# Optimization experiments

Measured on AMD Instinct MI355X. Metric: run time of the kernel, lower is better.

## Reference

```python
import jax, jax.numpy as jnp
import numpy as np

B, S, D = 4, 2048, 1024
H = 16
HD = D // H  # 64


def setup_inputs() -> dict:
    key = jax.random.key(0)
    ks = jax.random.split(key, 6)
    s = 0.02
    return {
        "x": jax.random.normal(ks[0], (B, S, D), dtype=jnp.float32),
        "w_q": jax.random.normal(ks[1], (D, D), dtype=jnp.float32) * s,
        "w_k": jax.random.normal(ks[2], (D, D), dtype=jnp.float32) * s,
        "w_v": jax.random.normal(ks[3], (D, D), dtype=jnp.float32) * s,
        "w_o": jax.random.normal(ks[4], (D, D), dtype=jnp.float32) * s,
        "b_o": jnp.zeros((D,), dtype=jnp.float32),
    }


def reference(x, w_q, w_k, w_v, w_o, b_o):
    b, n, d_in = x.shape
    # QKV projections (torch Linear: y = x @ W^T), reshape to heads
    q = (x @ w_q.T).reshape(b, n, H, HD).transpose(0, 2, 1, 3)  # [b,h,n,hd]
    k = (x @ w_k.T).reshape(b, n, H, HD).transpose(0, 2, 1, 3)
    v = (x @ w_v.T).reshape(b, n, H, HD).transpose(0, 2, 1, 3)
    scores = jnp.einsum("bhqd,bhkd->bhqk", q, k)
    causal = jnp.triu(jnp.ones((n, n), dtype=bool), k=1)  # True above diagonal -> masked
    scores = jnp.where(causal, -jnp.inf, scores)
    attn = jax.nn.softmax(scores / jnp.sqrt(jnp.float32(HD)), axis=-1)
    # dropout p=0.0 (no-op)
    ctx = jnp.einsum("bhqk,bhkd->bhqd", attn, v)
    ctx = ctx.transpose(0, 2, 1, 3).reshape(b, n, D)
    return ctx @ w_o.T + b_o
```

## Files before the change

### kernel.cpp

```cpp
#include <hip/hip_runtime.h>
#include <hip/hip_bf16.h>

typedef __bf16 bf16x8 __attribute__((ext_vector_type(8)));
typedef float f32x4 __attribute__((ext_vector_type(4)));
typedef unsigned short u16x4 __attribute__((ext_vector_type(4)));
typedef unsigned short u16x8 __attribute__((ext_vector_type(8)));

__device__ __forceinline__ unsigned short f2bf(float f) {
  unsigned int u = __float_as_uint(f);
  u += 0x7FFFu + ((u >> 16) & 1u);
  return (unsigned short)(u >> 16);
}

__device__ __forceinline__ float exp2_fast(float x) {
  return __builtin_amdgcn_exp2f(x);
}

__device__ __forceinline__ void gld_lds16(const void* g, void* l) {
  __builtin_amdgcn_global_load_lds(
      (__attribute__((address_space(1))) void*)g,
      (__attribute__((address_space(3))) void*)l,
      16, 0, 0);
}

__global__ __launch_bounds__(256)
void cvt_bf16(const float* __restrict__ x, const float* __restrict__ wq,
              const float* __restrict__ wk, const float* __restrict__ wv,
              const float* __restrict__ wo,
              unsigned short* __restrict__ Xb, unsigned short* __restrict__ Wb)
{
  unsigned c = blockIdx.x * 256 + threadIdx.x;
  const float* src;
  unsigned short* dst;
  unsigned off;
  if (c < 1048576u) {
    src = x; dst = Xb; off = c;
  } else {
    unsigned cc = c - 1048576u;
    unsigned which = cc >> 17;
    off = cc & 131071u;
    src = which == 0 ? wq : which == 1 ? wk : which == 2 ? wv : wo;
    dst = Wb + (size_t)which * 1048576u;
  }
  f32x4 a = *reinterpret_cast<const f32x4*>(src + (size_t)off * 8);
  f32x4 b = *reinterpret_cast<const f32x4*>(src + (size_t)off * 8 + 4);
  u16x8 o = {f2bf(a.x), f2bf(a.y), f2bf(a.z), f2bf(a.w),
             f2bf(b.x), f2bf(b.y), f2bf(b.z), f2bf(b.w)};
  *reinterpret_cast<u16x8*>(dst + (size_t)off * 8) = o;
}

__global__ __launch_bounds__(256, 3)
void qkv_proj_b(const unsigned short* __restrict__ Xb, const unsigned short* __restrict__ Wb,
                unsigned short* __restrict__ Qb, unsigned short* __restrict__ Kb,
                unsigned short* __restrict__ Vb)
{
  __shared__ __align__(16) unsigned short As[128 * 64];
  __shared__ __align__(16) unsigned short Bs[128 * 64];
  char* AsB = (char*)As;
  char* BsB = (char*)Bs;

  const int z = blockIdx.z;
  const unsigned short* __restrict__ W = Wb + (size_t)z * 1048576u;
  unsigned short* __restrict__ Out = (z == 0) ? Qb : (z == 1) ? Kb : Vb;

  const int flat = blockIdx.x + (blockIdx.y << 3);
  const int swz = (flat & 7) * 64 + (flat >> 3);
  const int n0 = (swz & 7) * 128;
  const int m0 = (swz >> 3) * 128;

  const int t = threadIdx.x;
  const int lane = t & 63, wid = t >> 6;
  const int wr = wid >> 1, wc = wid & 1;
  const int l15 = lane & 15, g = lane >> 4;

  f32x4 acc[4][4] = {};

  for (int kt = 0; kt < 1024; kt += 64) {
#pragma unroll
    for (int i = 0; i < 4; ++i) {
      const int rbase = wid * 32 + i * 8;
      const int row = rbase + (lane >> 3);
      const int swzb = ((lane & 7) * 16) ^ ((row & 7) << 4);
      gld_lds16((const char*)Xb + ((size_t)(m0 + row) * 1024 + kt) * 2 + swzb,
                AsB + rbase * 128);
      gld_lds16((const char*)W + ((size_t)(n0 + row) * 1024 + kt) * 2 + swzb,
                BsB + rbase * 128);
    }
    __syncthreads();

#pragma unroll
    for (int ks = 0; ks < 2; ++ks) {
      const int kpre = ks * 64 + g * 16;
      bf16x8 af[4], bfr[4];
#pragma unroll
      for (int mi = 0; mi < 4; ++mi) {
        int row = wr * 64 + mi * 16 + l15;
        af[mi] = *reinterpret_cast<const bf16x8*>(AsB + row * 128 + (kpre ^ ((row & 7) << 4)));
      }
#pragma unroll
      for (int ni = 0; ni < 4; ++ni) {
        int row = wc * 64 + ni * 16 + l15;
        bfr[ni] = *reinterpret_cast<const bf16x8*>(BsB + row * 128 + (kpre ^ ((row & 7) << 4)));
      }
#pragma unroll
      for (int mi = 0; mi < 4; ++mi)
#pragma unroll
        for (int ni = 0; ni < 4; ++ni)
          acc[mi][ni] = __builtin_amdgcn_mfma_f32_16x16x32_bf16(af[mi], bfr[ni], acc[mi][ni], 0, 0, 0);
    }
    __syncthreads();
  }

  if (z == 2) {
#pragma unroll
    for (int mi = 0; mi < 4; ++mi)
#pragma unroll
      for (int ni = 0; ni < 4; ++ni) {
        int n = n0 + wc * 64 + ni * 16 + l15;
        int h = n >> 6, hd = n & 63;
        int m = m0 + wr * 64 + mi * 16 + 4 * g;
        int b = m >> 11, s0 = m & 2047;
        u16x4 pk = {f2bf(acc[mi][ni][0]), f2bf(acc[mi][ni][1]),
                    f2bf(acc[mi][ni][2]), f2bf(acc[mi][ni][3])};
        *reinterpret_cast<u16x4*>(Out + ((size_t)(b * 16 + h) * 64 + hd) * 2048 + s0) = pk;
      }
  } else {
    const float qs = (z == 0) ? 0.1803368801f : 1.0f;
#pragma unroll
    for (int mi = 0; mi < 4; ++mi)
#pragma unroll
      for (int ni = 0; ni < 4; ++ni)
#pragma unroll
        for (int r = 0; r < 4; ++r) {
          int m = m0 + wr * 64 + mi * 16 + 4 * g + r;
          int n = n0 + wc * 64 + ni * 16 + l15;
          int b = m >> 11, s = m & 2047;
          int h = n >> 6, hd = n & 63;
          Out[((size_t)(b * 16 + h) * 2048 + s) * 64 + hd] = f2bf(acc[mi][ni][r] * qs);
        }
  }
}

__global__ __launch_bounds__(256, 3)
void out_proj_b(const unsigned short* __restrict__ Ctx, const unsigned short* __restrict__ Wob,
                const float* __restrict__ Bo, float* __restrict__ Y)
{
  __shared__ __align__(16) unsigned short As[128 * 64];
  __shared__ __align__(16) unsigned short Bs[128 * 64];
  char* AsB = (char*)As;
  char* BsB = (char*)Bs;

  const int flat = blockIdx.x + (blockIdx.y << 3);
  const int swz = (flat & 7) * 64 + (flat >> 3);
  const int n0 = (swz & 7) * 128;
  const int m0 = (swz >> 3) * 128;

  const int t = threadIdx.x;
  const int lane = t & 63, wid = t >> 6;
  const int wr = wid >> 1, wc = wid & 1;
  const int l15 = lane & 15, g = lane >> 4;

  f32x4 acc[4][4] = {};

  for (int kt = 0; kt < 1024; kt += 64) {
#pragma unroll
    for (int i = 0; i < 4; ++i) {
      const int rbase = wid * 32 + i * 8;
      const int row = rbase + (lane >> 3);
      const int swzb = ((lane & 7) * 16) ^ ((row & 7) << 4);
      gld_lds16((const char*)Ctx + ((size_t)(m0 + row) * 1024 + kt) * 2 + swzb,
                AsB + rbase * 128);
      gld_lds16((const char*)Wob + ((size_t)(n0 + row) * 1024 + kt) * 2 + swzb,
                BsB + rbase * 128);
    }
    __syncthreads();

#pragma unroll
    for (int ks = 0; ks < 2; ++ks) {
      const int kpre = ks * 64 + g * 16;
      bf16x8 af[4], bfr[4];
#pragma unroll
      for (int mi = 0; mi < 4; ++mi) {
        int row = wr * 64 + mi * 16 + l15;
        af[mi] = *reinterpret_cast<const bf16x8*>(AsB + row * 128 + (kpre ^ ((row & 7) << 4)));
      }
#pragma unroll
      for (int ni = 0; ni < 4; ++ni) {
        int row = wc * 64 + ni * 16 + l15;
        bfr[ni] = *reinterpret_cast<const bf16x8*>(BsB + row * 128 + (kpre ^ ((row & 7) << 4)));
      }
#pragma unroll
      for (int mi = 0; mi < 4; ++mi)
#pragma unroll
        for (int ni = 0; ni < 4; ++ni)
          acc[mi][ni] = __builtin_amdgcn_mfma_f32_16x16x32_bf16(af[mi], bfr[ni], acc[mi][ni], 0, 0, 0);
    }
    __syncthreads();
  }

#pragma unroll
  for (int mi = 0; mi < 4; ++mi)
#pragma unroll
    for (int ni = 0; ni < 4; ++ni) {
      int n = n0 + wc * 64 + ni * 16 + l15;
      float bias = Bo[n];
#pragma unroll
      for (int r = 0; r < 4; ++r) {
        int m = m0 + wr * 64 + mi * 16 + 4 * g + r;
        Y[(size_t)m * 1024 + n] = acc[mi][ni][r] + bias;
      }
    }
}

__global__ __launch_bounds__(256, 2)
void attn4(const unsigned short* __restrict__ Qb, const unsigned short* __restrict__ Kb,
           const unsigned short* __restrict__ Vtg, unsigned short* __restrict__ Ctx)
{
  __shared__ __align__(16) unsigned short Ks[2][64 * 64];
  __shared__ __align__(16) unsigned short Vts[2][64 * 64];
  __shared__ __align__(16) unsigned short Pl[4][64 * 64];

  const int flat = blockIdx.x;
  const int xcd = flat & 7;
  const int idx = flat >> 3;
  const int bh = xcd * 8 + (idx >> 3);
  const int tile = 7 - (idx & 7);

  const size_t base = (size_t)bh * (2048 * 64);
  const int lane = threadIdx.x & 63, wid = threadIdx.x >> 6;
  const int l15 = lane & 15, g = lane >> 4;
  char* PB = (char*)Pl[wid];
  const int bb = bh >> 4, hh = bh & 15;

  const int sl8 = lane >> 3;
  const int sc8 = lane & 7;
  const int pswz = (l15 & 7) << 4;

  const int qg0 = tile * 256 + wid * 64;
  const int nst = 4 * (tile + 1);

  bf16x8 qf[4][2];
#pragma unroll
  for (int mi = 0; mi < 4; ++mi)
#pragma unroll
    for (int ks = 0; ks < 2; ++ks)
      qf[mi][ks] = *reinterpret_cast<const bf16x8*>(
          Qb + base + (size_t)(qg0 + 16 * mi + l15) * 64 + ks * 32 + g * 8);

  bf16x8 ones;
#pragma unroll
  for (int i = 0; i < 8; ++i) ones[i] = (__bf16)1.0f;

  f32x4 o[4][4] = {};
  f32x4 accl[4] = {};

#pragma unroll
  for (int i = 0; i < 2; ++i) {
    int row = wid * 16 + i * 8 + sl8;
    int swzb = (sc8 * 16) ^ ((row & 7) << 4);
    gld_lds16((const char*)Kb + (base + (size_t)row * 64) * 2 + swzb,
              (char*)Ks[0] + (wid * 16 + i * 8) * 128);
    gld_lds16((const char*)Vtg + (base + (size_t)row * 2048) * 2 + swzb,
              (char*)Vts[0] + (wid * 16 + i * 8) * 128);
  }
  __syncthreads();

  int cur = 0;
  for (int s = 0; s < nst; ++s) {
    if (s + 1 < nst) {
#pragma unroll
      for (int i = 0; i < 2; ++i) {
        int row = wid * 16 + i * 8 + sl8;
        int swzb = (sc8 * 16) ^ ((row & 7) << 4);
        gld_lds16((const char*)Kb + (base + (size_t)((s + 1) * 64 + row) * 64) * 2 + swzb,
                  (char*)Ks[cur ^ 1] + (wid * 16 + i * 8) * 128);
        gld_lds16((const char*)Vtg + (base + (size_t)row * 2048 + (s + 1) * 64) * 2 + swzb,
                  (char*)Vts[cur ^ 1] + (wid * 16 + i * 8) * 128);
      }
    }
    char* KsB = (char*)Ks[cur];
    char* VtB = (char*)Vts[cur];

    f32x4 sw[4][4] = {};
#pragma unroll
    for (int ks = 0; ks < 2; ++ks) {
      const int kpre = ks * 64 + g * 16;
#pragma unroll
      for (int ni = 0; ni < 4; ++ni) {
        int row = ni * 16 + l15;
        bf16x8 kf = *reinterpret_cast<const bf16x8*>(KsB + row * 128 + (kpre ^ ((row & 7) << 4)));
#pragma unroll
        for (int mi = 0; mi < 4; ++mi)
          sw[mi][ni] = __builtin_amdgcn_mfma_f32_16x16x32_bf16(kf, qf[mi][ks], sw[mi][ni], 0, 0, 0);
      }
    }

    const bool needmask = (s * 64 + 63 > qg0);
    const int dgl = s * 64 + 4 * g - l15 - qg0;
#pragma unroll
    for (int mi = 0; mi < 4; ++mi) {
#pragma unroll
      for (int ni = 0; ni < 4; ++ni) {
        f32x4 v = sw[mi][ni];
        if (needmask) {
          int dbase = dgl + 16 * ni - 16 * mi;
#pragma unroll
          for (int r = 0; r < 4; ++r)
            if (dbase + r > 0) v[r] = -1e30f;
        }
        float p0 = exp2_fast(v[0]);
        float p1 = exp2_fast(v[1]);
        float p2 = exp2_fast(v[2]);
        float p3 = exp2_fast(v[3]);
        uint2 w;
        w.x = (__float_as_uint(p0) >> 16) | (__float_as_uint(p1) & 0xFFFF0000u);
        w.y = (__float_as_uint(p2) >> 16) | (__float_as_uint(p3) & 0xFFFF0000u);
        *reinterpret_cast<uint2*>(PB + (16 * mi + l15) * 128 + ((32 * ni + 8 * g) ^ pswz)) = w;
      }
    }
    asm volatile("s_waitcnt lgkmcnt(0)" ::: "memory");
    __builtin_amdgcn_sched_barrier(0);

#pragma unroll
    for (int ks2 = 0; ks2 < 2; ++ks2) {
      const int kpre = ks2 * 64 + g * 16;
      bf16x8 pa[4];
#pragma unroll
      for (int mi = 0; mi < 4; ++mi) {
        pa[mi] = *reinterpret_cast<const bf16x8*>(PB + (16 * mi + l15) * 128 + (kpre ^ pswz));
        accl[mi] = __builtin_amdgcn_mfma_f32_16x16x32_bf16(ones, pa[mi], accl[mi], 0, 0, 0);
      }
#pragma unroll
      for (int db = 0; db < 4; ++db) {
        int vrow = db * 16 + l15;
        bf16x8 vf = *reinterpret_cast<const bf16x8*>(VtB + vrow * 128 + (kpre ^ ((vrow & 7) << 4)));
#pragma unroll
        for (int mi = 0; mi < 4; ++mi)
          o[mi][db] = __builtin_amdgcn_mfma_f32_16x16x32_bf16(vf, pa[mi], o[mi][db], 0, 0, 0);
      }
    }
    __syncthreads();
    cur ^= 1;
  }

#pragma unroll
  for (int mi = 0; mi < 4; ++mi) {
    float inv = 1.0f / accl[mi][0];
    int qg = qg0 + 16 * mi + l15;
#pragma unroll
    for (int db = 0; db < 4; ++db) {
      u16x4 pk = {f2bf(o[mi][db][0] * inv), f2bf(o[mi][db][1] * inv),
                  f2bf(o[mi][db][2] * inv), f2bf(o[mi][db][3] * inv)};
      *reinterpret_cast<u16x4*>(Ctx + ((size_t)(bb * 2048 + qg)) * 1024 + hh * 64 + db * 16 + 4 * g) = pk;
    }
  }
}

__global__ __launch_bounds__(256, 2)
void qkv_proj(const float* __restrict__ X,
              const float* __restrict__ Wq, const float* __restrict__ Wk,
              const float* __restrict__ Wv,
              unsigned short* __restrict__ Qb, unsigned short* __restrict__ Kb,
              unsigned short* __restrict__ Vb)
{
  __shared__ __align__(16) unsigned short As[128 * 64];
  __shared__ __align__(16) unsigned short Bs[128 * 64];
  char* AsB = (char*)As;
  char* BsB = (char*)Bs;

  const float* __restrict__ W =
      (blockIdx.z == 0) ? Wq : (blockIdx.z == 1) ? Wk : Wv;
  unsigned short* __restrict__ Out =
      (blockIdx.z == 0) ? Qb : (blockIdx.z == 1) ? Kb : Vb;

  const int m0 = blockIdx.y * 128;
  const int n0 = blockIdx.x * 128;
  const int t = threadIdx.x;
  const int lane = t & 63, wid = t >> 6;
  const int wr = wid >> 1, wc = wid & 1;
  const int l15 = lane & 15, g = lane >> 4;

  f32x4 acc[4][4] = {};

  for (int kt = 0; kt < 1024; kt += 64) {
#pragma unroll
    for (int i = 0; i < 8; ++i) {
      int c = i * 256 + t;
      int row = c >> 4, c4 = c & 15;
      f32x4 a = *reinterpret_cast<const f32x4*>(X + (size_t)(m0 + row) * 1024 + kt + c4 * 4);
      f32x4 b = *reinterpret_cast<const f32x4*>(W + (size_t)(n0 + row) * 1024 + kt + c4 * 4);
      u16x4 va = {f2bf(a.x), f2bf(a.y), f2bf(a.z), f2bf(a.w)};
      u16x4 vb = {f2bf(b.x), f2bf(b.y), f2bf(b.z), f2bf(b.w)};
      int off = row * 128 + ((c4 * 8) ^ ((row & 7) << 4));
      *reinterpret_cast<u16x4*>(AsB + off) = va;
      *reinterpret_cast<u16x4*>(BsB + off) = vb;
    }
    __syncthreads();

#pragma unroll
    for (int ks = 0; ks < 2; ++ks) {
      const int kpre = ks * 64 + g * 16;
      bf16x8 af[4], bfr[4];
#pragma unroll
      for (int mi = 0; mi < 4; ++mi) {
        int row = wr * 64 + mi * 16 + l15;
        af[mi] = *reinterpret_cast<const bf16x8*>(AsB + row * 128 + (kpre ^ ((row & 7) << 4)));
      }
#pragma unroll
      for (int ni = 0; ni < 4; ++ni) {
        int row = wc * 64 + ni * 16 + l15;
        bfr[ni] = *reinterpret_cast<const bf16x8*>(BsB + row * 128 + (kpre ^ ((row & 7) << 4)));
      }
#pragma unroll
      for (int mi = 0; mi < 4; ++mi)
#pragma unroll
        for (int ni = 0; ni < 4; ++ni)
          acc[mi][ni] = __builtin_amdgcn_mfma_f32_16x16x32_bf16(af[mi], bfr[ni], acc[mi][ni], 0, 0, 0);
    }
    __syncthreads();
  }

  if (blockIdx.z == 2) {
#pragma unroll
    for (int mi = 0; mi < 4; ++mi)
#pragma unroll
      for (int ni = 0; ni < 4; ++ni) {
        int n = n0 + wc * 64 + ni * 16 + l15;
        int h = n >> 6, hd = n & 63;
        int m = m0 + wr * 64 + mi * 16 + 4 * g;
        int b = m >> 11, s0 = m & 2047;
        u16x4 pk = {f2bf(acc[mi][ni][0]), f2bf(acc[mi][ni][1]),
                    f2bf(acc[mi][ni][2]), f2bf(acc[mi][ni][3])};
        *reinterpret_cast<u16x4*>(Out + ((size_t)(b * 16 + h) * 64 + hd) * 2048 + s0) = pk;
      }
  } else {
    const float qs = (blockIdx.z == 0) ? 0.1803368801f : 1.0f;
#pragma unroll
    for (int mi = 0; mi < 4; ++mi)
#pragma unroll
      for (int ni = 0; ni < 4; ++ni)
#pragma unroll
        for (int r = 0; r < 4; ++r) {
          int m = m0 + wr * 64 + mi * 16 + 4 * g + r;
          int n = n0 + wc * 64 + ni * 16 + l15;
          int b = m >> 11, s = m & 2047;
          int h = n >> 6, hd = n & 63;
          Out[((size_t)(b * 16 + h) * 2048 + s) * 64 + hd] = f2bf(acc[mi][ni][r] * qs);
        }
  }
}

__global__ __launch_bounds__(256, 2)
void out_proj(const unsigned short* __restrict__ Ctx, const float* __restrict__ Wo,
              const float* __restrict__ Bo, float* __restrict__ Y)
{
  __shared__ __align__(16) unsigned short As[128 * 64];
  __shared__ __align__(16) unsigned short Bs[128 * 64];
  char* AsB = (char*)As;
  char* BsB = (char*)Bs;

  const int m0 = blockIdx.y * 128;
  const int n0 = blockIdx.x * 128;
  const int t = threadIdx.x;
  const int lane = t & 63, wid = t >> 6;
  const int wr = wid >> 1, wc = wid & 1;
  const int l15 = lane & 15, g = lane >> 4;

  f32x4 acc[4][4] = {};

  for (int kt = 0; kt < 1024; kt += 64) {
#pragma unroll
    for (int i = 0; i < 4; ++i) {
      int c = i * 256 + t;
      int row = c >> 3, c8 = c & 7;
      bf16x8 v = *reinterpret_cast<const bf16x8*>(Ctx + (size_t)(m0 + row) * 1024 + kt + c8 * 8);
      *reinterpret_cast<bf16x8*>(AsB + row * 128 + ((c8 * 16) ^ ((row & 7) << 4))) = v;
    }
#pragma unroll
    for (int i = 0; i < 8; ++i) {
      int c = i * 256 + t;
      int row = c >> 4, c4 = c & 15;
      f32x4 b = *reinterpret_cast<const f32x4*>(Wo + (size_t)(n0 + row) * 1024 + kt + c4 * 4);
      u16x4 vb = {f2bf(b.x), f2bf(b.y), f2bf(b.z), f2bf(b.w)};
      *reinterpret_cast<u16x4*>(BsB + row * 128 + ((c4 * 8) ^ ((row & 7) << 4))) = vb;
    }
    __syncthreads();

#pragma unroll
    for (int ks = 0; ks < 2; ++ks) {
      const int kpre = ks * 64 + g * 16;
      bf16x8 af[4], bfr[4];
#pragma unroll
      for (int mi = 0; mi < 4; ++mi) {
        int row = wr * 64 + mi * 16 + l15;
        af[mi] = *reinterpret_cast<const bf16x8*>(AsB + row * 128 + (kpre ^ ((row & 7) << 4)));
      }
#pragma unroll
      for (int ni = 0; ni < 4; ++ni) {
        int row = wc * 64 + ni * 16 + l15;
        bfr[ni] = *reinterpret_cast<const bf16x8*>(BsB + row * 128 + (kpre ^ ((row & 7) << 4)));
      }
#pragma unroll
      for (int mi = 0; mi < 4; ++mi)
#pragma unroll
        for (int ni = 0; ni < 4; ++ni)
          acc[mi][ni] = __builtin_amdgcn_mfma_f32_16x16x32_bf16(af[mi], bfr[ni], acc[mi][ni], 0, 0, 0);
    }
    __syncthreads();
  }

#pragma unroll
  for (int mi = 0; mi < 4; ++mi)
#pragma unroll
    for (int ni = 0; ni < 4; ++ni) {
      int n = n0 + wc * 64 + ni * 16 + l15;
      float bias = Bo[n];
#pragma unroll
      for (int r = 0; r < 4; ++r) {
        int m = m0 + wr * 64 + mi * 16 + 4 * g + r;
        Y[(size_t)m * 1024 + n] = acc[mi][ni][r] + bias;
      }
    }
}

extern "C" void kernel_launch(void* const* d_in, const int* in_sizes, int n_in,
                              void* d_out, int out_size, void* d_ws, size_t ws_size,
                              hipStream_t stream)
{
  const float* x  = (const float*)d_in[0];
  const float* wq = (const float*)d_in[1];
  const float* wk = (const float*)d_in[2];
  const float* wv = (const float*)d_in[3];
  const float* wo = (const float*)d_in[4];
  const float* bo = (const float*)d_in[5];
  float* y = (float*)d_out;

  if (ws_size >= 75497472ULL) {
    unsigned short* Xb = (unsigned short*)d_ws;
    unsigned short* Qb = Xb + 8388608;
    unsigned short* Kb = Qb + 8388608;
    unsigned short* Vb = Kb + 8388608;
    unsigned short* Wb = Vb + 8388608;
    unsigned short* Cx = Xb;

    cvt_bf16<<<6144, 256, 0, stream>>>(x, wq, wk, wv, wo, Xb, Wb);
    qkv_proj_b<<<dim3(8, 64, 3), 256, 0, stream>>>(Xb, Wb, Qb, Kb, Vb);
    attn4<<<512, 256, 0, stream>>>(Qb, Kb, Vb, Cx);
    out_proj_b<<<dim3(8, 64), 256, 0, stream>>>(Cx, Wb + 3 * 1048576, bo, y);
  } else {
    unsigned short* Qb = (unsigned short*)d_ws;
    unsigned short* Kb = Qb + 8388608;
    unsigned short* Vb = Kb + 8388608;
    unsigned short* Cx = Vb + 8388608;

    qkv_proj<<<dim3(8, 64, 3), 256, 0, stream>>>(x, wq, wk, wv, Qb, Kb, Vb);
    attn4<<<512, 256, 0, stream>>>(Qb, Kb, Vb, Cx);
    out_proj<<<dim3(8, 64), 256, 0, stream>>>(Cx, wo, bo, y);
  }
}
```

Baseline: 185.8 us.

## Pair causal query tiles per block to balance attention work

```diff
diff --git a/kernel.cpp b/kernel.cpp
--- a/kernel.cpp
+++ b/kernel.cpp
@@ -14,6 +14,10 @@
 
 __device__ __forceinline__ float exp2_fast(float x) {
   return __builtin_amdgcn_exp2f(x);
+}
+
+__device__ __forceinline__ unsigned pack_bf16(float lo, float hi) {
+  return __builtin_amdgcn_perm(__float_as_uint(hi), __float_as_uint(lo), 0x07060302u);
 }
 
 __device__ __forceinline__ void gld_lds16(const void* g, void* l) {
@@ -213,21 +217,22 @@
 }
 
 __global__ __launch_bounds__(256, 2)
-void attn4(const unsigned short* __restrict__ Qb, const unsigned short* __restrict__ Kb,
+void attn2(const unsigned short* __restrict__ Qb, const unsigned short* __restrict__ Kb,
            const unsigned short* __restrict__ Vtg, unsigned short* __restrict__ Ctx)
 {
   __shared__ __align__(16) unsigned short Ks[2][64 * 64];
   __shared__ __align__(16) unsigned short Vts[2][64 * 64];
-  __shared__ __align__(16) unsigned short Pl[4][64 * 64];
+  __shared__ __align__(16) unsigned short Pl[4][32 * 64];
 
   const int flat = blockIdx.x;
   const int xcd = flat & 7;
   const int idx = flat >> 3;
   const int bh = xcd * 8 + (idx >> 3);
-  const int tile = 7 - (idx & 7);
+  const int pr = idx & 7;
 
   const size_t base = (size_t)bh * (2048 * 64);
-  const int lane = threadIdx.x & 63, wid = threadIdx.x >> 6;
+  const int t = threadIdx.x;
+  const int lane = t & 63, wid = t >> 6;
   const int l15 = lane & 15, g = lane >> 4;
   char* PB = (char*)Pl[wid];
   const int bb = bh >> 4, hh = bh & 15;
@@ -236,122 +241,121 @@
   const int sc8 = lane & 7;
   const int pswz = (l15 & 7) << 4;
 
-  const int qg0 = tile * 256 + wid * 64;
-  const int nst = 4 * (tile + 1);
-
-  bf16x8 qf[4][2];
-#pragma unroll
-  for (int mi = 0; mi < 4; ++mi)
-#pragma unroll
-    for (int ks = 0; ks < 2; ++ks)
-      qf[mi][ks] = *reinterpret_cast<const bf16x8*>(
-          Qb + base + (size_t)(qg0 + 16 * mi + l15) * 64 + ks * 32 + g * 8);
-
   bf16x8 ones;
 #pragma unroll
   for (int i = 0; i < 8; ++i) ones[i] = (__bf16)1.0f;
 
-  f32x4 o[4][4] = {};
-  f32x4 accl[4] = {};
-
-#pragma unroll
-  for (int i = 0; i < 2; ++i) {
-    int row = wid * 16 + i * 8 + sl8;
-    int swzb = (sc8 * 16) ^ ((row & 7) << 4);
-    gld_lds16((const char*)Kb + (base + (size_t)row * 64) * 2 + swzb,
-              (char*)Ks[0] + (wid * 16 + i * 8) * 128);
-    gld_lds16((const char*)Vtg + (base + (size_t)row * 2048) * 2 + swzb,
-              (char*)Vts[0] + (wid * 16 + i * 8) * 128);
-  }
-  __syncthreads();
-
-  int cur = 0;
-  for (int s = 0; s < nst; ++s) {
-    if (s + 1 < nst) {
-#pragma unroll
-      for (int i = 0; i < 2; ++i) {
-        int row = wid * 16 + i * 8 + sl8;
-        int swzb = (sc8 * 16) ^ ((row & 7) << 4);
-        gld_lds16((const char*)Kb + (base + (size_t)((s + 1) * 64 + row) * 64) * 2 + swzb,
-                  (char*)Ks[cur ^ 1] + (wid * 16 + i * 8) * 128);
-        gld_lds16((const char*)Vtg + (base + (size_t)row * 2048 + (s + 1) * 64) * 2 + swzb,
-                  (char*)Vts[cur ^ 1] + (wid * 16 + i * 8) * 128);
-      }
-    }
-    char* KsB = (char*)Ks[cur];
-    char* VtB = (char*)Vts[cur];
-
-    f32x4 sw[4][4] = {};
-#pragma unroll
-    for (int ks = 0; ks < 2; ++ks) {
-      const int kpre = ks * 64 + g * 16;
-#pragma unroll
-      for (int ni = 0; ni < 4; ++ni) {
-        int row = ni * 16 + l15;
-        bf16x8 kf = *reinterpret_cast<const bf16x8*>(KsB + row * 128 + (kpre ^ ((row & 7) << 4)));
-#pragma unroll
-        for (int mi = 0; mi < 4; ++mi)
-          sw[mi][ni] = __builtin_amdgcn_mfma_f32_16x16x32_bf16(kf, qf[mi][ks], sw[mi][ni], 0, 0, 0);
-      }
-    }
-
-    const bool needmask = (s * 64 + 63 > qg0);
-    const int dgl = s * 64 + 4 * g - l15 - qg0;
-#pragma unroll
-    for (int mi = 0; mi < 4; ++mi) {
-#pragma unroll
-      for (int ni = 0; ni < 4; ++ni) {
-        f32x4 v = sw[mi][ni];
-        if (needmask) {
-          int dbase = dgl + 16 * ni - 16 * mi;
-#pragma unroll
-          for (int r = 0; r < 4; ++r)
-            if (dbase + r > 0) v[r] = -1e30f;
+  for (int half = 0; half < 2; ++half) {
+    const int tile = half ? (15 - pr) : pr;
+    const int qg0 = tile * 128 + wid * 32;
+    const int nst = 2 * tile + 2;
+
+    bf16x8 qf[2][2];
+#pragma unroll
+    for (int mi = 0; mi < 2; ++mi)
+#pragma unroll
+      for (int ks = 0; ks < 2; ++ks)
+        qf[mi][ks] = *reinterpret_cast<const bf16x8*>(
+            Qb + base + (size_t)(qg0 + 16 * mi + l15) * 64 + ks * 32 + g * 8);
+
+    f32x4 o[2][4] = {};
+    f32x4 accl[2] = {};
+
+#pragma unroll
+    for (int i = 0; i < 2; ++i) {
+      int row = wid * 16 + i * 8 + sl8;
+      int swzb = (sc8 * 16) ^ ((row & 7) << 4);
+      gld_lds16((const char*)Kb + (base + (size_t)row * 64) * 2 + swzb,
+                (char*)Ks[0] + (wid * 16 + i * 8) * 128);
+      gld_lds16((const char*)Vtg + (base + (size_t)row * 2048) * 2 + swzb,
+                (char*)Vts[0] + (wid * 16 + i * 8) * 128);
+    }
+    __syncthreads();
+
+    int cur = 0;
+    for (int s = 0; s < nst; ++s) {
+      if (s + 1 < nst) {
+#pragma unroll
+        for (int i = 0; i < 2; ++i) {
+          int row = wid * 16 + i * 8 + sl8;
+          int swzb = (sc8 * 16) ^ ((row & 7) << 4);
+          gld_lds16((const char*)Kb + (base + (size_t)((s + 1) * 64 + row) * 64) * 2 + swzb,
+                    (char*)Ks[cur ^ 1] + (wid * 16 + i * 8) * 128);
+          gld_lds16((const char*)Vtg + (base + (size_t)row * 2048 + (s + 1) * 64) * 2 + swzb,
+                    (char*)Vts[cur ^ 1] + (wid * 16 + i * 8) * 128);
         }
-        float p0 = exp2_fast(v[0]);
-        float p1 = exp2_fast(v[1]);
-        float p2 = exp2_fast(v[2]);
-        float p3 = exp2_fast(v[3]);
-        uint2 w;
-        w.x = (__float_as_uint(p0) >> 16) | (__float_as_uint(p1) & 0xFFFF0000u);
-        w.y = (__float_as_uint(p2) >> 16) | (__float_as_uint(p3) & 0xFFFF0000u);
-        *reinterpret_cast<uint2*>(PB + (16 * mi + l15) * 128 + ((32 * ni + 8 * g) ^ pswz)) = w;
-      }
-    }
-    asm volatile("s_waitcnt lgkmcnt(0)" ::: "memory");
-    __builtin_amdgcn_sched_barrier(0);
-
-#pragma unroll
-    for (int ks2 = 0; ks2 < 2; ++ks2) {
-      const int kpre = ks2 * 64 + g * 16;
-      bf16x8 pa[4];
-#pragma unroll
-      for (int mi = 0; mi < 4; ++mi) {
-        pa[mi] = *reinterpret_cast<const bf16x8*>(PB + (16 * mi + l15) * 128 + (kpre ^ pswz));
-        accl[mi] = __builtin_amdgcn_mfma_f32_16x16x32_bf16(ones, pa[mi], accl[mi], 0, 0, 0);
-      }
+      }
+      char* KsB = (char*)Ks[cur];
+      char* VtB = (char*)Vts[cur];
+
+      f32x4 sw[2][4] = {};
+#pragma unroll
+      for (int ks = 0; ks < 2; ++ks) {
+        const int kpre = ks * 64 + g * 16;
+#pragma unroll
+        for (int ni = 0; ni < 4; ++ni) {
+          int row = ni * 16 + l15;
+          bf16x8 kf = *reinterpret_cast<const bf16x8*>(KsB + row * 128 + (kpre ^ ((row & 7) << 4)));
+          sw[0][ni] = __builtin_amdgcn_mfma_f32_16x16x32_bf16(kf, qf[0][ks], sw[0][ni], 0, 0, 0);
+          sw[1][ni] = __builtin_amdgcn_mfma_f32_16x16x32_bf16(kf, qf[1][ks], sw[1][ni], 0, 0, 0);
+        }
+      }
+
+      const bool needmask = (s * 64 + 63 > qg0);
+      const int dgl = s * 64 + 4 * g - l15 - qg0;
+#pragma unroll
+      for (int mi = 0; mi < 2; ++mi) {
+#pragma unroll
+        for (int ni = 0; ni < 4; ++ni) {
+          f32x4 v = sw[mi][ni];
+          if (needmask) {
+            int dbase = dgl + 16 * ni - 16 * mi;
+#pragma unroll
+            for (int r = 0; r < 4; ++r)
+              if (dbase + r > 0) v[r] = -1e30f;
+          }
+          float p0 = exp2_fast(v[0]);
+          float p1 = exp2_fast(v[1]);
+          float p2 = exp2_fast(v[2]);
+          float p3 = exp2_fast(v[3]);
+          uint2 w;
+          w.x = pack_bf16(p0, p1);
+          w.y = pack_bf16(p2, p3);
+          *reinterpret_cast<uint2*>(PB + (16 * mi + l15) * 128 + ((32 * ni + 8 * g) ^ pswz)) = w;
+        }
+      }
+      asm volatile("s_waitcnt lgkmcnt(0)" ::: "memory");
+      __builtin_amdgcn_sched_barrier(0);
+
+#pragma unroll
+      for (int ks2 = 0; ks2 < 2; ++ks2) {
+        const int kpre = ks2 * 64 + g * 16;
+        bf16x8 pa0 = *reinterpret_cast<const bf16x8*>(PB + l15 * 128 + (kpre ^ pswz));
+        bf16x8 pa1 = *reinterpret_cast<const bf16x8*>(PB + (16 + l15) * 128 + (kpre ^ pswz));
+        accl[0] = __builtin_amdgcn_mfma_f32_16x16x32_bf16(ones, pa0, accl[0], 0, 0, 0);
+        accl[1] = __builtin_amdgcn_mfma_f32_16x16x32_bf16(ones, pa1, accl[1], 0, 0, 0);
+#pragma unroll
+        for (int db = 0; db < 4; ++db) {
+          int vrow = db * 16 + l15;
+          bf16x8 vf = *reinterpret_cast<const bf16x8*>(VtB + vrow * 128 + (kpre ^ ((vrow & 7) << 4)));
+          o[0][db] = __builtin_amdgcn_mfma_f32_16x16x32_bf16(vf, pa0, o[0][db], 0, 0, 0);
+          o[1][db] = __builtin_amdgcn_mfma_f32_16x16x32_bf16(vf, pa1, o[1][db], 0, 0, 0);
+        }
+      }
+      __syncthreads();
+      cur ^= 1;
+    }
+
+#pragma unroll
+    for (int mi = 0; mi < 2; ++mi) {
+      float inv = 1.0f / accl[mi][0];
+      int qg = qg0 + 16 * mi + l15;
 #pragma unroll
       for (int db = 0; db < 4; ++db) {
-        int vrow = db * 16 + l15;
-        bf16x8 vf = *reinterpret_cast<const bf16x8*>(VtB + vrow * 128 + (kpre ^ ((vrow & 7) << 4)));
-#pragma unroll
-        for (int mi = 0; mi < 4; ++mi)
-          o[mi][db] = __builtin_amdgcn_mfma_f32_16x16x32_bf16(vf, pa[mi], o[mi][db], 0, 0, 0);
-      }
-    }
-    __syncthreads();
-    cur ^= 1;
-  }
-
-#pragma unroll
-  for (int mi = 0; mi < 4; ++mi) {
-    float inv = 1.0f / accl[mi][0];
-    int qg = qg0 + 16 * mi + l15;
-#pragma unroll
-    for (int db = 0; db < 4; ++db) {
-      u16x4 pk = {f2bf(o[mi][db][0] * inv), f2bf(o[mi][db][1] * inv),
-                  f2bf(o[mi][db][2] * inv), f2bf(o[mi][db][3] * inv)};
-      *reinterpret_cast<u16x4*>(Ctx + ((size_t)(bb * 2048 + qg)) * 1024 + hh * 64 + db * 16 + 4 * g) = pk;
+        u16x4 pk = {f2bf(o[mi][db][0] * inv), f2bf(o[mi][db][1] * inv),
+                    f2bf(o[mi][db][2] * inv), f2bf(o[mi][db][3] * inv)};
+        *reinterpret_cast<u16x4*>(Ctx + ((size_t)(bb * 2048 + qg)) * 1024 + hh * 64 + db * 16 + 4 * g) = pk;
+      }
     }
   }
 }
@@ -545,7 +549,7 @@
 
     cvt_bf16<<<6144, 256, 0, stream>>>(x, wq, wk, wv, wo, Xb, Wb);
     qkv_proj_b<<<dim3(8, 64, 3), 256, 0, stream>>>(Xb, Wb, Qb, Kb, Vb);
-    attn4<<<512, 256, 0, stream>>>(Qb, Kb, Vb, Cx);
+    attn2<<<512, 256, 0, stream>>>(Qb, Kb, Vb, Cx);
     out_proj_b<<<dim3(8, 64), 256, 0, stream>>>(Cx, Wb + 3 * 1048576, bo, y);
   } else {
     unsigned short* Qb = (unsigned short*)d_ws;
@@ -554,7 +558,7 @@
     unsigned short* Cx = Vb + 8388608;
 
     qkv_proj<<<dim3(8, 64, 3), 256, 0, stream>>>(x, wq, wk, wv, Qb, Kb, Vb);
-    attn4<<<512, 256, 0, stream>>>(Qb, Kb, Vb, Cx);
+    attn2<<<512, 256, 0, stream>>>(Qb, Kb, Vb, Cx);
     out_proj<<<dim3(8, 64), 256, 0, stream>>>(Cx, wo, bo, y);
   }
 }
```

Result: faster. 151.3 us (-18.6%).
